# Kernel tuning notes

Measured on AMD Instinct MI355X. Metric: run time of the kernel, lower is better.

The kernel has to match this reference:

```python
import jax, jax.numpy as jnp
import numpy as np
from jax import lax

SIGMOID_THRESH = 0.05


def setup_inputs() -> dict:
    key = jax.random.key(0)
    # [B, num_kps, H, W] raw (pre-sigmoid) heatmap logits
    heatmaps = jax.random.normal(key, (16, 17, 512, 512), dtype=jnp.float32)
    return {"heatmaps": heatmaps, "kernel_size": 3}


def reference(heatmaps, kernel_size):
    # Faithful to Heatmaps.get_local_max_coords, expressed as a dense mask
    # (torch.nonzero has a data-dependent output shape, so we return the
    # masked peak scores instead of the coordinate list; the coordinate
    # extraction is a trivial host-side nonzero on the mask).
    assert kernel_size % 2 == 1
    pad = kernel_size // 2
    # max_pool2d(kernel_size, stride=1, padding=kernel_size//2)
    max_heatmaps = lax.reduce_window(
        heatmaps,
        -jnp.inf,
        lax.max,
        window_dimensions=(1, 1, kernel_size, kernel_size),
        window_strides=(1, 1, 1, 1),
        padding=((0, 0), (0, 0), (pad, pad), (pad, pad)),
    )
    scores = jax.nn.sigmoid(heatmaps)
    keep = (max_heatmaps == heatmaps) & (scores > SIGMOID_THRESH)
    # peak score map: nonzero entries are exactly the coords torch.nonzero
    # would return, with the peak confidence as the value.
    return jnp.where(keep, scores, jnp.zeros((), dtype=heatmaps.dtype))
```

## Files before the change

kernel.cpp:

```cpp
#include <hip/hip_runtime.h>
#include <math.h>

#define HM_W 512
#define HM_H 512
#define TILE_ROWS 4
#define LDS_STRIDE 516
#define SIG_THRESH 0.05f

__global__ __launch_bounds__(512) void heatmap_peak_kernel(
    const float* __restrict__ in, float* __restrict__ out) {
    __shared__ float s[TILE_ROWS + 2][LDS_STRIDE];

    const int tx = threadIdx.x;
    const int ty = threadIdx.y;
    const int t  = ty * 128 + tx;
    const int y0 = blockIdx.y * TILE_ROWS;
    const long long base = (long long)blockIdx.z * (HM_H * HM_W);

    for (int i = t; i < (TILE_ROWS + 2) * 128; i += 512) {
        const int r  = i >> 7;
        const int c  = i & 127;
        const int gy = y0 - 1 + r;
        float4 v;
        if (gy >= 0 && gy < HM_H) {
            v = ((const float4*)(in + base + (long long)gy * HM_W))[c];
        } else {
            v = make_float4(-INFINITY, -INFINITY, -INFINITY, -INFINITY);
        }
        *(float4*)&s[r][c * 4] = v;
    }
    __syncthreads();

    const int x0 = tx * 4;
    const float4 r0 = *(const float4*)&s[ty][x0];
    const float4 r1 = *(const float4*)&s[ty + 1][x0];
    const float4 r2 = *(const float4*)&s[ty + 2][x0];

    float4 vm;
    vm.x = fmaxf(fmaxf(r0.x, r1.x), r2.x);
    vm.y = fmaxf(fmaxf(r0.y, r1.y), r2.y);
    vm.z = fmaxf(fmaxf(r0.z, r1.z), r2.z);
    vm.w = fmaxf(fmaxf(r0.w, r1.w), r2.w);

    const float left = (x0 == 0) ? -INFINITY
        : fmaxf(fmaxf(s[ty][x0 - 1], s[ty + 1][x0 - 1]), s[ty + 2][x0 - 1]);
    const float right = (x0 + 4 >= HM_W) ? -INFINITY
        : fmaxf(fmaxf(s[ty][x0 + 4], s[ty + 1][x0 + 4]), s[ty + 2][x0 + 4]);

    float4 hm;
    hm.x = fmaxf(left, fmaxf(vm.x, vm.y));
    hm.y = fmaxf(vm.x, fmaxf(vm.y, vm.z));
    hm.z = fmaxf(vm.y, fmaxf(vm.z, vm.w));
    hm.w = fmaxf(vm.z, fmaxf(vm.w, right));

    float4 o;
    {
        const float sc = 1.0f / (1.0f + expf(-r1.x));
        o.x = (hm.x == r1.x && sc > SIG_THRESH) ? sc : 0.0f;
    }
    {
        const float sc = 1.0f / (1.0f + expf(-r1.y));
        o.y = (hm.y == r1.y && sc > SIG_THRESH) ? sc : 0.0f;
    }
    {
        const float sc = 1.0f / (1.0f + expf(-r1.z));
        o.z = (hm.z == r1.z && sc > SIG_THRESH) ? sc : 0.0f;
    }
    {
        const float sc = 1.0f / (1.0f + expf(-r1.w));
        o.w = (hm.w == r1.w && sc > SIG_THRESH) ? sc : 0.0f;
    }

    ((float4*)(out + base + (long long)(y0 + ty) * HM_W))[tx] = o;
}

extern "C" void kernel_launch(void* const* d_in, const int* in_sizes, int n_in,
                              void* d_out, int out_size, void* d_ws, size_t ws_size,
                              hipStream_t stream) {
    const float* heatmaps = (const float*)d_in[0];
    float* out = (float*)d_out;

    const int planes = in_sizes[0] / (HM_H * HM_W);

    dim3 block(128, TILE_ROWS, 1);
    dim3 grid(1, HM_H / TILE_ROWS, planes);
    heatmap_peak_kernel<<<grid, block, 0, stream>>>(heatmaps, out);
}
```

Before: 447.1 us.

## Process four rows per thread with register row reuse and larger tiles

Enlarges each block's tile to 16 output rows and has each thread sweep four consecutive rows, rotating the 3-row vertical window in registers. This cuts the halo reload overhead from 50% to 12.5% and reduces LDS reads per output. It also switches to the fast __expf intrinsic and nontemporal output stores. The fast exp can slightly change sigmoid values near the threshold.

```diff
diff --git a/kernel.cpp b/kernel.cpp
--- a/kernel.cpp
+++ b/kernel.cpp
@@ -3,13 +3,16 @@
 
 #define HM_W 512
 #define HM_H 512
-#define TILE_ROWS 4
+#define TILE_ROWS 16
+#define HALO_ROWS (TILE_ROWS + 2)
 #define LDS_STRIDE 516
 #define SIG_THRESH 0.05f
 
+typedef float f32x4 __attribute__((ext_vector_type(4)));
+
 __global__ __launch_bounds__(512) void heatmap_peak_kernel(
     const float* __restrict__ in, float* __restrict__ out) {
-    __shared__ float s[TILE_ROWS + 2][LDS_STRIDE];
+    __shared__ float s[HALO_ROWS][LDS_STRIDE];
 
     const int tx = threadIdx.x;
     const int ty = threadIdx.y;
@@ -17,7 +20,7 @@
     const int y0 = blockIdx.y * TILE_ROWS;
     const long long base = (long long)blockIdx.z * (HM_H * HM_W);
 
-    for (int i = t; i < (TILE_ROWS + 2) * 128; i += 512) {
+    for (int i = t; i < HALO_ROWS * 128; i += 512) {
         const int r  = i >> 7;
         const int c  = i & 127;
         const int gy = y0 - 1 + r;
@@ -31,47 +34,64 @@
     }
     __syncthreads();
 
-    const int x0 = tx * 4;
-    const float4 r0 = *(const float4*)&s[ty][x0];
-    const float4 r1 = *(const float4*)&s[ty + 1][x0];
-    const float4 r2 = *(const float4*)&s[ty + 2][x0];
+    const int x0   = tx * 4;
+    const int row0 = ty * 4;
+    const bool has_l = (x0 != 0);
+    const bool has_r = (x0 + 4 < HM_W);
 
-    float4 vm;
-    vm.x = fmaxf(fmaxf(r0.x, r1.x), r2.x);
-    vm.y = fmaxf(fmaxf(r0.y, r1.y), r2.y);
-    vm.z = fmaxf(fmaxf(r0.z, r1.z), r2.z);
-    vm.w = fmaxf(fmaxf(r0.w, r1.w), r2.w);
+    float4 a = *(const float4*)&s[row0][x0];
+    float4 b = *(const float4*)&s[row0 + 1][x0];
+    float la = has_l ? s[row0][x0 - 1]     : -INFINITY;
+    float lb = has_l ? s[row0 + 1][x0 - 1] : -INFINITY;
+    float ra = has_r ? s[row0][x0 + 4]     : -INFINITY;
+    float rb = has_r ? s[row0 + 1][x0 + 4] : -INFINITY;
 
-    const float left = (x0 == 0) ? -INFINITY
-        : fmaxf(fmaxf(s[ty][x0 - 1], s[ty + 1][x0 - 1]), s[ty + 2][x0 - 1]);
-    const float right = (x0 + 4 >= HM_W) ? -INFINITY
-        : fmaxf(fmaxf(s[ty][x0 + 4], s[ty + 1][x0 + 4]), s[ty + 2][x0 + 4]);
+    #pragma unroll
+    for (int k = 0; k < 4; ++k) {
+        const int rr = row0 + k;
+        const float4 c4 = *(const float4*)&s[rr + 2][x0];
+        const float  lc = has_l ? s[rr + 2][x0 - 1] : -INFINITY;
+        const float  rc = has_r ? s[rr + 2][x0 + 4] : -INFINITY;
 
-    float4 hm;
-    hm.x = fmaxf(left, fmaxf(vm.x, vm.y));
-    hm.y = fmaxf(vm.x, fmaxf(vm.y, vm.z));
-    hm.z = fmaxf(vm.y, fmaxf(vm.z, vm.w));
-    hm.w = fmaxf(vm.z, fmaxf(vm.w, right));
+        float4 vm;
+        vm.x = fmaxf(fmaxf(a.x, b.x), c4.x);
+        vm.y = fmaxf(fmaxf(a.y, b.y), c4.y);
+        vm.z = fmaxf(fmaxf(a.z, b.z), c4.z);
+        vm.w = fmaxf(fmaxf(a.w, b.w), c4.w);
+        const float lm = fmaxf(fmaxf(la, lb), lc);
+        const float rm = fmaxf(fmaxf(ra, rb), rc);
 
-    float4 o;
-    {
-        const float sc = 1.0f / (1.0f + expf(-r1.x));
-        o.x = (hm.x == r1.x && sc > SIG_THRESH) ? sc : 0.0f;
+        float4 hm;
+        hm.x = fmaxf(lm,   fmaxf(vm.x, vm.y));
+        hm.y = fmaxf(vm.x, fmaxf(vm.y, vm.z));
+        hm.z = fmaxf(vm.y, fmaxf(vm.z, vm.w));
+        hm.w = fmaxf(vm.z, fmaxf(vm.w, rm));
+
+        f32x4 o;
+        {
+            const float sc = 1.0f / (1.0f + __expf(-b.x));
+            o.x = (hm.x == b.x && sc > SIG_THRESH) ? sc : 0.0f;
+        }
+        {
+            const float sc = 1.0f / (1.0f + __expf(-b.y));
+            o.y = (hm.y == b.y && sc > SIG_THRESH) ? sc : 0.0f;
+        }
+        {
+            const float sc = 1.0f / (1.0f + __expf(-b.z));
+            o.z = (hm.z == b.z && sc > SIG_THRESH) ? sc : 0.0f;
+        }
+        {
+            const float sc = 1.0f / (1.0f + __expf(-b.w));
+            o.w = (hm.w == b.w && sc > SIG_THRESH) ? sc : 0.0f;
+        }
+
+        f32x4* optr = (f32x4*)(out + base + (long long)(y0 + rr) * HM_W) + tx;
+        __builtin_nontemporal_store(o, optr);
+
+        a = b; b = c4;
+        la = lb; lb = lc;
+        ra = rb; rb = rc;
     }
-    {
-        const float sc = 1.0f / (1.0f + expf(-r1.y));
-        o.y = (hm.y == r1.y && sc > SIG_THRESH) ? sc : 0.0f;
-    }
-    {
-        const float sc = 1.0f / (1.0f + expf(-r1.z));
-        o.z = (hm.z == r1.z && sc > SIG_THRESH) ? sc : 0.0f;
-    }
-    {
-        const float sc = 1.0f / (1.0f + expf(-r1.w));
-        o.w = (hm.w == r1.w && sc > SIG_THRESH) ? sc : 0.0f;
-    }
-
-    ((float4*)(out + base + (long long)(y0 + ty) * HM_W))[tx] = o;
 }
 
 extern "C" void kernel_launch(void* const* d_in, const int* in_sizes, int n_in,
@@ -82,7 +102,7 @@
 
     const int planes = in_sizes[0] / (HM_H * HM_W);
 
-    dim3 block(128, TILE_ROWS, 1);
+    dim3 block(128, 4, 1);
     dim3 grid(1, HM_H / TILE_ROWS, planes);
     heatmap_peak_kernel<<<grid, block, 0, stream>>>(heatmaps, out);
 }
```

New measurement: 474.7 us. 1.06x slower.
